# Optimization experiments

Measured on AMD Instinct MI355X. Metric: run time of the kernel, lower is better.

The kernel has to match this reference:

```python
import jax, jax.numpy as jnp
import numpy as np

B, C, H, W = 8, 512, 96, 96
CQ = C // 8


def setup_inputs() -> dict:
    key = jax.random.key(0)
    ks = jax.random.split(key, 8)
    s = 1.0 / np.sqrt(C)  # conv-like init scale to keep logits sane
    return {
        "x": jax.random.normal(ks[0], (B, C, H, W), jnp.float32),
        "Wq": jax.random.normal(ks[1], (CQ, C), jnp.float32) * s,
        "bq": jax.random.normal(ks[2], (CQ,), jnp.float32) * s,
        "Wk": jax.random.normal(ks[3], (CQ, C), jnp.float32) * s,
        "bk": jax.random.normal(ks[4], (CQ,), jnp.float32) * s,
        "Wv": jax.random.normal(ks[5], (C, C), jnp.float32) * s,
        "bv": jax.random.normal(ks[6], (C,), jnp.float32) * s,
        "gamma": jax.random.normal(ks[7], (1,), jnp.float32),
    }


def reference(x, Wq, bq, Wk, bk, Wv, bv, gamma):
    # 1x1 convs == per-pixel linear projections
    q = jnp.einsum('bchw,oc->bohw', x, Wq) + bq[None, :, None, None]  # [B,CQ,H,W]
    k = jnp.einsum('bchw,oc->bohw', x, Wk) + bk[None, :, None, None]  # [B,CQ,H,W]
    v = jnp.einsum('bchw,oc->bohw', x, Wv) + bv[None, :, None, None]  # [B,C ,H,W]

    h = x.shape[2]
    # column (vertical) attention logits: query at (h,w) vs keys at (j,w)
    energy_H = jnp.einsum('bchw,bcjw->bhwj', q, k)  # [B,H,W,H]
    # row (horizontal) attention logits: query at (h,w) vs keys at (h,j)
    energy_W = jnp.einsum('bchw,bchj->bhwj', q, k)  # [B,H,W,W]

    att = jax.nn.softmax(jnp.concatenate([energy_H, energy_W], axis=-1), axis=-1)
    att_H = att[..., :h]   # [B,H,W,H]
    att_W = att[..., h:]   # [B,H,W,W]

    out_H = jnp.einsum('bcjw,bhwj->bchw', v, att_H)
    out_W = jnp.einsum('bchj,bhwj->bchw', v, att_W)
    return gamma[0] * (out_H + out_W)
```

## Files before the change

kernel.cpp:

```cpp
#include <hip/hip_runtime.h>

#define B 8
#define C 512
#define H 96
#define W 96
#define HW (H*W)
#define KD 512
#define NSP 9216

typedef __attribute__((ext_vector_type(4))) float f32x4;
typedef __attribute__((ext_vector_type(8))) _Float16 f16x8;

typedef __attribute__((address_space(3))) unsigned int lds_u32;
typedef const __attribute__((address_space(1))) unsigned int glb_u32;
static __device__ __forceinline__ void gload16(const void* gsrc, void* ldst) {
    __builtin_amdgcn_global_load_lds((glb_u32*)gsrc, (lds_u32*)ldst, 16, 0, 0);
}

static __device__ __forceinline__ int tidx(int row, int kgrp) {
    return row * 32 + ((kgrp ^ ((row >> 2) & 3)) << 3);
}
static __device__ __forceinline__ int tidx64(int row, int gr) {
    return row * 64 + ((gr ^ (row & 7)) << 3);
}

__global__ __launch_bounds__(256) void split_w(
    const float* __restrict__ Wv, const float* __restrict__ Wq, const float* __restrict__ Wk,
    _Float16* __restrict__ Wv_h,
    _Float16* __restrict__ Wqk_h, _Float16* __restrict__ Wqk_l)
{
    int i = blockIdx.x * 256 + threadIdx.x;
    if (i < C * C) Wv_h[i] = (_Float16)Wv[i];
    if (i < 128 * C) {
        int m = i / C, k = i % C;
        float f = (m < 64) ? Wq[m * C + k] : Wk[(m - 64) * C + k];
        _Float16 h = (_Float16)f;
        Wqk_h[i] = h;
        Wqk_l[i] = (_Float16)(f - (float)h);
    }
}

__global__ __launch_bounds__(256) void split_x(
    const float* __restrict__ x,
    _Float16* __restrict__ xhT, _Float16* __restrict__ xlT)
{
    __shared__ float t[64][65];
    int n0 = blockIdx.x * 64, k0 = blockIdx.y * 64, b = blockIdx.z;
    int tid = threadIdx.x;
    const float* xb = x + ((size_t)b * KD + k0) * NSP + n0;
    #pragma unroll
    for (int it = 0; it < 16; ++it) {
        int idx = tid + it * 256;
        t[idx >> 6][idx & 63] = xb[(size_t)(idx >> 6) * NSP + (idx & 63)];
    }
    __syncthreads();
    #pragma unroll
    for (int it = 0; it < 2; ++it) {
        int gid = tid + it * 256;
        int n = gid >> 3, g = gid & 7;
        f16x8 hi, lo;
        #pragma unroll
        for (int u = 0; u < 8; ++u) {
            float f = t[g * 8 + u][n];
            _Float16 hh = (_Float16)f;
            hi[u] = hh;
            lo[u] = (_Float16)(f - (float)hh);
        }
        size_t off = ((size_t)b * NSP + n0 + n) * KD + k0 + g * 8;
        *(f16x8*)&xhT[off] = hi;
        *(f16x8*)&xlT[off] = lo;
    }
}

__global__ __launch_bounds__(256, 2) void gemm_v(
    const _Float16* __restrict__ xhT,
    const _Float16* __restrict__ Wh,
    const float* __restrict__ bias,
    _Float16* __restrict__ out16)
{
    __shared__ _Float16 smem[8192];
    const int W_OFF = 0, X_OFF = 4096;

    int tid = threadIdx.x;
    int n0 = blockIdx.x * 128, m0 = blockIdx.y * 128, b = blockIdx.z;
    int lane = tid & 63, wave = tid >> 6;
    int wr = wave >> 1, wc = wave & 1;
    int l15 = lane & 15, l4 = lane >> 4;

    int grow = tid >> 2, gcol = (tid & 3) * 8;
    const _Float16* pW = Wh + (size_t)(m0 + grow) * KD + gcol;
    const _Float16* pX = xhT + ((size_t)b * NSP + n0 + grow) * KD + gcol;
    const size_t half = (size_t)64 * KD;
    int ldsW0 = W_OFF + wave * 512;
    int ldsW1 = W_OFF + 2048 + wave * 512;
    int ldsX0 = X_OFF + wave * 512;
    int ldsX1 = X_OFF + 2048 + wave * 512;

    f32x4 acc[4][4];
    #pragma unroll
    for (int i = 0; i < 4; ++i)
        #pragma unroll
        for (int j = 0; j < 4; ++j)
            acc[i][j] = (f32x4){0.f, 0.f, 0.f, 0.f};

    for (int k0 = 0; k0 < KD; k0 += 32) {
        gload16(pW + k0,        &smem[ldsW0]);
        gload16(pW + half + k0, &smem[ldsW1]);
        gload16(pX + k0,        &smem[ldsX0]);
        gload16(pX + half + k0, &smem[ldsX1]);
        __syncthreads();

        f16x8 af[4], bf[4];
        #pragma unroll
        for (int f = 0; f < 4; ++f) {
            af[f] = *(const f16x8*)&smem[W_OFF + (wr * 64 + f * 16 + l15) * 32 + l4 * 8];
            bf[f] = *(const f16x8*)&smem[X_OFF + (wc * 64 + f * 16 + l15) * 32 + l4 * 8];
        }
        #pragma unroll
        for (int i = 0; i < 4; ++i)
            #pragma unroll
            for (int j = 0; j < 4; ++j)
                acc[i][j] = __builtin_amdgcn_mfma_f32_16x16x32_f16(af[i], bf[j], acc[i][j], 0, 0, 0);
        __syncthreads();
    }

    #pragma unroll
    for (int i = 0; i < 4; ++i)
        #pragma unroll
        for (int r = 0; r < 4; ++r) {
            int row = m0 + wr * 64 + i * 16 + l4 * 4 + r;
            float bv = bias[row];
            #pragma unroll
            for (int j = 0; j < 4; ++j) {
                int col = n0 + wc * 64 + j * 16 + l15;
                out16[((size_t)b * C + row) * NSP + col] = (_Float16)(acc[i][j][r] + bv);
            }
        }
}

__global__ __launch_bounds__(256, 2) void gemm_qk(
    const _Float16* __restrict__ xhT, const _Float16* __restrict__ xlT,
    const _Float16* __restrict__ Wqh, const _Float16* __restrict__ Wql,
    const float* __restrict__ bias0, const float* __restrict__ bias1,
    _Float16* __restrict__ qh, _Float16* __restrict__ ql,
    _Float16* __restrict__ kh, _Float16* __restrict__ kl)
{
    __shared__ _Float16 smem[16384];
    const int XH = 0, XL = 4096, WHo = 8192, WLo = 12288;

    int tid = threadIdx.x;
    int n0 = blockIdx.x * 128, b = blockIdx.z;
    int lane = tid & 63, wave = tid >> 6;
    int wr = wave >> 1, wc = wave & 1;
    int l15 = lane & 15, l4 = lane >> 4;

    int grow = tid >> 2, gcol = (tid & 3) * 8;
    const _Float16* pXh = xhT + ((size_t)b * NSP + n0 + grow) * KD + gcol;
    const _Float16* pXl = xlT + ((size_t)b * NSP + n0 + grow) * KD + gcol;
    const _Float16* pWh = Wqh + (size_t)grow * KD + gcol;
    const _Float16* pWl = Wql + (size_t)grow * KD + gcol;
    const size_t half = (size_t)64 * KD;
    int base0 = wave * 512, base1 = 2048 + wave * 512;

    f32x4 acc[4][4];
    #pragma unroll
    for (int i = 0; i < 4; ++i)
        #pragma unroll
        for (int j = 0; j < 4; ++j)
            acc[i][j] = (f32x4){0.f, 0.f, 0.f, 0.f};

    for (int k0 = 0; k0 < KD; k0 += 32) {
        gload16(pXh + k0,        &smem[XH + base0]);
        gload16(pXh + half + k0, &smem[XH + base1]);
        gload16(pXl + k0,        &smem[XL + base0]);
        gload16(pXl + half + k0, &smem[XL + base1]);
        gload16(pWh + k0,        &smem[WHo + base0]);
        gload16(pWh + half + k0, &smem[WHo + base1]);
        gload16(pWl + k0,        &smem[WLo + base0]);
        gload16(pWl + half + k0, &smem[WLo + base1]);
        __syncthreads();

        f16x8 axh[4], axl[4], bwh[4], bwl[4];
        #pragma unroll
        for (int f = 0; f < 4; ++f) {
            int ra = (wr * 64 + f * 16 + l15) * 32 + l4 * 8;
            int rb = (wc * 64 + f * 16 + l15) * 32 + l4 * 8;
            axh[f] = *(const f16x8*)&smem[XH + ra];
            axl[f] = *(const f16x8*)&smem[XL + ra];
            bwh[f] = *(const f16x8*)&smem[WHo + rb];
            bwl[f] = *(const f16x8*)&smem[WLo + rb];
        }
        #pragma unroll
        for (int i = 0; i < 4; ++i)
            #pragma unroll
            for (int j = 0; j < 4; ++j)
                acc[i][j] = __builtin_amdgcn_mfma_f32_16x16x32_f16(axh[i], bwh[j], acc[i][j], 0, 0, 0);
        #pragma unroll
        for (int i = 0; i < 4; ++i)
            #pragma unroll
            for (int j = 0; j < 4; ++j)
                acc[i][j] = __builtin_amdgcn_mfma_f32_16x16x32_f16(axh[i], bwl[j], acc[i][j], 0, 0, 0);
        #pragma unroll
        for (int i = 0; i < 4; ++i)
            #pragma unroll
            for (int j = 0; j < 4; ++j)
                acc[i][j] = __builtin_amdgcn_mfma_f32_16x16x32_f16(axl[i], bwh[j], acc[i][j], 0, 0, 0);
        __syncthreads();
    }

    #pragma unroll
    for (int i = 0; i < 4; ++i)
        #pragma unroll
        for (int r = 0; r < 4; ++r) {
            int sp = n0 + wr * 64 + i * 16 + l4 * 4 + r;
            #pragma unroll
            for (int j = 0; j < 4; ++j) {
                int wcol = wc * 64 + j * 16 + l15;
                float val = acc[i][j][r] + (wcol < 64 ? bias0[wcol] : bias1[wcol - 64]);
                _Float16 hi = (_Float16)val;
                _Float16 lo = (_Float16)(val - (float)hi);
                size_t off = ((size_t)b * NSP + sp) * 64 + (wcol & 63);
                if (wcol < 64) { qh[off] = hi; ql[off] = lo; }
                else           { kh[off] = hi; kl[off] = lo; }
            }
        }
}

__global__ __launch_bounds__(256, 2) void energy_mfma(
    const _Float16* __restrict__ qh, const _Float16* __restrict__ ql,
    const _Float16* __restrict__ kh, const _Float16* __restrict__ kl,
    float* __restrict__ out, int pMul, int rMul)
{
    __shared__ _Float16 sm[4 * 96 * 64];
    const int T_QH = 0, T_QL = 6144, T_KH = 12288, T_KL = 18432;
    int p = blockIdx.x, b = blockIdx.y;
    int tid = threadIdx.x;
    size_t base = ((size_t)b * HW + (size_t)p * pMul) * 64;
    size_t rstride = (size_t)rMul * 64;

    #pragma unroll
    for (int tile = 0; tile < 4; ++tile) {
        const _Float16* src = (tile == 0) ? qh : (tile == 1) ? ql : (tile == 2) ? kh : kl;
        int tb = tile * 6144;
        #pragma unroll
        for (int sub = 0; sub < 3; ++sub) {
            int s = sub * 256 + tid;
            int row = s >> 3, g = s & 7;
            f16x8 d = *(const f16x8*)&src[base + row * rstride + g * 8];
            *(f16x8*)&sm[tb + tidx64(row, g)] = d;
        }
    }
    __syncthreads();

    int lane = tid & 63, wave = tid >> 6;
    int wr = wave >> 1, wc = wave & 1;
    int l15 = lane & 15, l4 = lane >> 4;

    f32x4 acc[3][3];
    #pragma unroll
    for (int i = 0; i < 3; ++i)
        #pragma unroll
        for (int j = 0; j < 3; ++j)
            acc[i][j] = (f32x4){0.f, 0.f, 0.f, 0.f};

    #pragma unroll
    for (int ks = 0; ks < 2; ++ks) {
        f16x8 Ah[3], Al[3], Bh[3], Bl[3];
        int gr = ks * 4 + l4;
        #pragma unroll
        for (int i = 0; i < 3; ++i) {
            int sa = tidx64(wr * 48 + i * 16 + l15, gr);
            Ah[i] = *(const f16x8*)&sm[T_QH + sa];
            Al[i] = *(const f16x8*)&sm[T_QL + sa];
            int sb = tidx64(wc * 48 + i * 16 + l15, gr);
            Bh[i] = *(const f16x8*)&sm[T_KH + sb];
            Bl[i] = *(const f16x8*)&sm[T_KL + sb];
        }
        #pragma unroll
        for (int i = 0; i < 3; ++i)
            #pragma unroll
            for (int j = 0; j < 3; ++j) {
                acc[i][j] = __builtin_amdgcn_mfma_f32_16x16x32_f16(Ah[i], Bh[j], acc[i][j], 0, 0, 0);
                acc[i][j] = __builtin_amdgcn_mfma_f32_16x16x32_f16(Ah[i], Bl[j], acc[i][j], 0, 0, 0);
                acc[i][j] = __builtin_amdgcn_mfma_f32_16x16x32_f16(Al[i], Bh[j], acc[i][j], 0, 0, 0);
            }
    }

    size_t ob = (size_t)(b * 96 + p) * 9216;
    #pragma unroll
    for (int i = 0; i < 3; ++i)
        #pragma unroll
        for (int r = 0; r < 4; ++r) {
            int row = wr * 48 + i * 16 + l4 * 4 + r;
            #pragma unroll
            for (int j = 0; j < 3; ++j)
                out[ob + (size_t)row * 96 + wc * 48 + j * 16 + l15] = acc[i][j][r];
        }
}

__global__ __launch_bounds__(256) void maxsum(
    const float* __restrict__ EW, const float* __restrict__ EH,
    const float* __restrict__ gamma, float* __restrict__ ms)
{
    int gw = (blockIdx.x * 256 + threadIdx.x) >> 6;
    int lane = threadIdx.x & 63;
    int b = gw / HW, hw = gw % HW;
    int h = hw / 96, w = hw % 96;
    const float* ew = &EW[((size_t)(b * 96 + h) * 96 + w) * 96];
    const float* eh = &EH[((size_t)(b * 96 + w) * 96 + h) * 96];
    float v0 = ew[lane];
    float v1 = (lane < 32) ? ew[64 + lane] : eh[lane - 32];
    float v2 = eh[32 + lane];
    float m = fmaxf(fmaxf(v0, v1), v2);
    #pragma unroll
    for (int s = 32; s; s >>= 1) m = fmaxf(m, __shfl_xor(m, s));
    float pp = __expf(v0 - m) + __expf(v1 - m) + __expf(v2 - m);
    #pragma unroll
    for (int s = 32; s; s >>= 1) pp += __shfl_xor(pp, s);
    if (lane == 0) {
        ms[(size_t)gw * 2]     = m;
        ms[(size_t)gw * 2 + 1] = gamma[0] / pp;
    }
}

template<int OUT16>
__global__ __launch_bounds__(256) void agg_mfma(
    const float* __restrict__ E, const float* __restrict__ ms,
    const _Float16* __restrict__ v16,
    float* __restrict__ dstF, _Float16* __restrict__ dstH, int msMode)
{
    __shared__ _Float16 satt[3][96 * 32];

    int r = blockIdx.x, b = blockIdx.y;
    int tid = threadIdx.x;
    int lane = tid & 63, wave = tid >> 6;
    int l15 = lane & 15, l4 = lane >> 4;

    const float* Eb = &E[(size_t)(b * 96 + r) * 9216];
    int msBase = b * HW;
    #pragma unroll
    for (int it = 0; it < 5; ++it) {
        int g_id = tid + it * 256;
        if (g_id < 1152) {
            int s = g_id / 12, gj = g_id % 12;
            int mi = msMode ? (msBase + s * 96 + r) : (msBase + r * 96 + s);
            float m  = ms[(size_t)mi * 2];
            float sc = ms[(size_t)mi * 2 + 1];
            float4 e0 = *(const float4*)&Eb[s * 96 + gj * 8];
            float4 e1 = *(const float4*)&Eb[s * 96 + gj * 8 + 4];
            float pv[8] = {e0.x, e0.y, e0.z, e0.w, e1.x, e1.y, e1.z, e1.w};
            f16x8 ph;
            #pragma unroll
            for (int u = 0; u < 8; ++u)
                ph[u] = (_Float16)(__expf(pv[u] - m) * sc);
            *(f16x8*)&satt[gj >> 2][tidx(s, gj & 3)] = ph;
        }
    }
    __syncthreads();

    const _Float16* vb = v16 + (size_t)b * C * 9216 + r * 96;

    for (int cc = 0; cc < 4; ++cc) {
        int cbase = cc * 128 + wave * 32;
        f32x4 acc[2][6];
        #pragma unroll
        for (int i = 0; i < 2; ++i)
            #pragma unroll
            for (int n = 0; n < 6; ++n)
                acc[i][n] = (f32x4){0.f, 0.f, 0.f, 0.f};

        #pragma unroll
        for (int kc = 0; kc < 3; ++kc) {
            f16x8 af[2];
            #pragma unroll
            for (int i = 0; i < 2; ++i)
                af[i] = *(const f16x8*)&vb[(size_t)(cbase + i * 16 + l15) * 9216 + kc * 32 + l4 * 8];
            f16x8 Bp[6];
            #pragma unroll
            for (int n = 0; n < 6; ++n)
                Bp[n] = *(const f16x8*)&satt[kc][tidx(n * 16 + l15, l4)];
            #pragma unroll
            for (int i = 0; i < 2; ++i)
                #pragma unroll
                for (int n = 0; n < 6; ++n)
                    acc[i][n] = __builtin_amdgcn_mfma_f32_16x16x32_f16(af[i], Bp[n], acc[i][n], 0, 0, 0);
        }

        #pragma unroll
        for (int i = 0; i < 2; ++i)
            #pragma unroll
            for (int r4 = 0; r4 < 4; ++r4) {
                int cl = cbase + i * 16 + l4 * 4 + r4;
                size_t rowb = ((size_t)b * C + cl) * 9216 + r * 96;
                #pragma unroll
                for (int n = 0; n < 6; ++n) {
                    int s = n * 16 + l15;
                    if (OUT16) dstH[rowb + s] = (_Float16)acc[i][n][r4];
                    else       dstF[rowb + s] = acc[i][n][r4];
                }
            }
    }
}

__global__ __launch_bounds__(256) void transpose_f16(
    const _Float16* __restrict__ src, _Float16* __restrict__ dst)
{
    size_t base = (size_t)blockIdx.x * (96 * 96);
    __shared__ _Float16 t[96][97];
    int tid = threadIdx.x;
    for (int i = tid; i < 96 * 96; i += 256) t[i / 96][i % 96] = src[base + i];
    __syncthreads();
    for (int i = tid; i < 96 * 96; i += 256) dst[base + i] = t[i % 96][i / 96];
}

__global__ __launch_bounds__(256) void transpose_add(
    const _Float16* __restrict__ srcT, float* __restrict__ out)
{
    size_t base = (size_t)blockIdx.x * (96 * 96);
    __shared__ _Float16 t[96][97];
    int tid = threadIdx.x;
    for (int i = tid; i < 96 * 96; i += 256) t[i / 96][i % 96] = srcT[base + i];
    __syncthreads();
    for (int i = tid; i < 96 * 96; i += 256) out[base + i] += (float)t[i % 96][i / 96];
}

__global__ __launch_bounds__(256) void combine(
    const _Float16* __restrict__ w16, const _Float16* __restrict__ hT,
    float* __restrict__ out)
{
    size_t base = (size_t)blockIdx.x * (96 * 96);
    __shared__ _Float16 t[96][97];
    int tid = threadIdx.x;
    for (int i = tid; i < 96 * 96; i += 256) t[i / 96][i % 96] = hT[base + i];
    __syncthreads();
    for (int i = tid; i < 96 * 96; i += 256)
        out[base + i] = (float)w16[base + i] + (float)t[i % 96][i / 96];
}

extern "C" void kernel_launch(void* const* d_in, const int* in_sizes, int n_in,
                              void* d_out, int out_size, void* d_ws, size_t ws_size,
                              hipStream_t stream)
{
    const float* x     = (const float*)d_in[0];
    const float* Wq    = (const float*)d_in[1];
    const float* bq    = (const float*)d_in[2];
    const float* Wk    = (const float*)d_in[3];
    const float* bk    = (const float*)d_in[4];
    const float* Wv    = (const float*)d_in[5];
    const float* bv    = (const float*)d_in[6];
    const float* gamma = (const float*)d_in[7];
    float* out = (float*)d_out;

    const size_t NK = (size_t)B * NSP * KD;
    _Float16* xhT = (_Float16*)d_ws;
    _Float16* xlT = xhT + NK;
    _Float16* qh  = xlT + NK;
    _Float16* ql  = qh + (size_t)B * HW * 64;
    _Float16* kh  = ql + (size_t)B * HW * 64;
    _Float16* kl  = kh + (size_t)B * HW * 64;
    float* EHp = (float*)(kl + (size_t)B * HW * 64);
    float* EWp = EHp + (size_t)B * HW * 96;
    float* ms  = (float*)qh;
    _Float16* vA  = xlT;
    _Float16* vB  = xhT;
    _Float16* outHT = xlT;

    _Float16* Wv_h  = (_Float16*)EHp;
    _Float16* Wqk_h = Wv_h + (size_t)C * C;
    _Float16* Wqk_l = Wqk_h + (size_t)128 * C;

    const size_t NEED = 245366784ull;
    bool bigws = ws_size >= NEED + NK * sizeof(_Float16);
    _Float16* outW16 = (_Float16*)((char*)d_ws + NEED);

    dim3 blk(256);

    split_w<<<dim3((C*C + 255)/256), blk, 0, stream>>>(Wv, Wq, Wk, Wv_h, Wqk_h, Wqk_l);
    split_x<<<dim3(NSP/64, KD/64, B), blk, 0, stream>>>(x, xhT, xlT);

    gemm_qk<<<dim3(NSP/128, 1, B), blk, 0, stream>>>(xhT, xlT, Wqk_h, Wqk_l, bq, bk, qh, ql, kh, kl);
    gemm_v<<<dim3(NSP/128, C/128, B), blk, 0, stream>>>(xhT, Wv_h, bv, vA);

    energy_mfma<<<dim3(96, B), blk, 0, stream>>>(qh, ql, kh, kl, EWp, 96, 1);
    energy_mfma<<<dim3(96, B), blk, 0, stream>>>(qh, ql, kh, kl, EHp, 1, 96);

    maxsum<<<dim3(B*HW/4), blk, 0, stream>>>(EWp, EHp, gamma, ms);

    transpose_f16<<<dim3(B*C), blk, 0, stream>>>(vA, vB);

    if (bigws) {
        agg_mfma<1><<<dim3(96, B), blk, 0, stream>>>(EWp, ms, vA, nullptr, outW16, 0);
        agg_mfma<1><<<dim3(96, B), blk, 0, stream>>>(EHp, ms, vB, nullptr, outHT, 1);
        combine<<<dim3(B*C), blk, 0, stream>>>(outW16, outHT, out);
    } else {
        agg_mfma<0><<<dim3(96, B), blk, 0, stream>>>(EWp, ms, vA, out, nullptr, 0);
        agg_mfma<1><<<dim3(96, B), blk, 0, stream>>>(EHp, ms, vB, nullptr, outHT, 1);
        transpose_add<<<dim3(B*C), blk, 0, stream>>>(outHT, out);
    }
}
```

Before: 382.1 us.

## Fuse softmax max/sum partials into energy kernel and vectorize split_x loads

```diff
diff --git a/kernel.cpp b/kernel.cpp
--- a/kernel.cpp
+++ b/kernel.cpp
@@ -49,9 +49,14 @@
     int tid = threadIdx.x;
     const float* xb = x + ((size_t)b * KD + k0) * NSP + n0;
     #pragma unroll
-    for (int it = 0; it < 16; ++it) {
+    for (int it = 0; it < 4; ++it) {
         int idx = tid + it * 256;
-        t[idx >> 6][idx & 63] = xb[(size_t)(idx >> 6) * NSP + (idx & 63)];
+        int kr = idx >> 4, nq = idx & 15;
+        float4 v = *(const float4*)&xb[(size_t)kr * NSP + nq * 4];
+        t[kr][nq * 4 + 0] = v.x;
+        t[kr][nq * 4 + 1] = v.y;
+        t[kr][nq * 4 + 2] = v.z;
+        t[kr][nq * 4 + 3] = v.w;
     }
     __syncthreads();
     #pragma unroll
@@ -229,7 +234,7 @@
 __global__ __launch_bounds__(256, 2) void energy_mfma(
     const _Float16* __restrict__ qh, const _Float16* __restrict__ ql,
     const _Float16* __restrict__ kh, const _Float16* __restrict__ kl,
-    float* __restrict__ out, int pMul, int rMul)
+    float* __restrict__ out, float* __restrict__ part, int pMul, int rMul)
 {
     __shared__ _Float16 sm[4 * 96 * 64];
     const int T_QH = 0, T_QL = 6144, T_KH = 12288, T_KL = 18432;
@@ -296,31 +301,49 @@
             for (int j = 0; j < 3; ++j)
                 out[ob + (size_t)row * 96 + wc * 48 + j * 16 + l15] = acc[i][j][r];
         }
-}
-
-__global__ __launch_bounds__(256) void maxsum(
-    const float* __restrict__ EW, const float* __restrict__ EH,
+
+    __syncthreads();
+    float* scr = (float*)sm;
+    #pragma unroll
+    for (int i = 0; i < 3; ++i)
+        #pragma unroll
+        for (int r = 0; r < 4; ++r) {
+            int row = wr * 48 + i * 16 + l4 * 4 + r;
+            float m3 = fmaxf(fmaxf(acc[i][0][r], acc[i][1][r]), acc[i][2][r]);
+            #pragma unroll
+            for (int mk = 1; mk < 16; mk <<= 1) m3 = fmaxf(m3, __shfl_xor(m3, mk));
+            float s = __expf(acc[i][0][r] - m3) + __expf(acc[i][1][r] - m3) + __expf(acc[i][2][r] - m3);
+            #pragma unroll
+            for (int mk = 1; mk < 16; mk <<= 1) s += __shfl_xor(s, mk);
+            if (l15 == 0) {
+                scr[row * 4 + wc * 2]     = m3;
+                scr[row * 4 + wc * 2 + 1] = s;
+            }
+        }
+    __syncthreads();
+    if (tid < 96) {
+        float m0 = scr[tid * 4], s0 = scr[tid * 4 + 1];
+        float m1 = scr[tid * 4 + 2], s1 = scr[tid * 4 + 3];
+        float M = fmaxf(m0, m1);
+        float S = s0 * __expf(m0 - M) + s1 * __expf(m1 - M);
+        size_t idx = (pMul == 96) ? ((size_t)b * HW + p * 96 + tid)
+                                  : ((size_t)b * HW + tid * 96 + p);
+        part[idx * 2]     = M;
+        part[idx * 2 + 1] = S;
+    }
+}
+
+__global__ __launch_bounds__(256) void combine_ms(
+    const float* __restrict__ pW, const float* __restrict__ pH,
     const float* __restrict__ gamma, float* __restrict__ ms)
 {
-    int gw = (blockIdx.x * 256 + threadIdx.x) >> 6;
-    int lane = threadIdx.x & 63;
-    int b = gw / HW, hw = gw % HW;
-    int h = hw / 96, w = hw % 96;
-    const float* ew = &EW[((size_t)(b * 96 + h) * 96 + w) * 96];
-    const float* eh = &EH[((size_t)(b * 96 + w) * 96 + h) * 96];
-    float v0 = ew[lane];
-    float v1 = (lane < 32) ? ew[64 + lane] : eh[lane - 32];
-    float v2 = eh[32 + lane];
-    float m = fmaxf(fmaxf(v0, v1), v2);
-    #pragma unroll
-    for (int s = 32; s; s >>= 1) m = fmaxf(m, __shfl_xor(m, s));
-    float pp = __expf(v0 - m) + __expf(v1 - m) + __expf(v2 - m);
-    #pragma unroll
-    for (int s = 32; s; s >>= 1) pp += __shfl_xor(pp, s);
-    if (lane == 0) {
-        ms[(size_t)gw * 2]     = m;
-        ms[(size_t)gw * 2 + 1] = gamma[0] / pp;
-    }
+    int row = blockIdx.x * 256 + threadIdx.x;
+    float mW = pW[row * 2], sW = pW[row * 2 + 1];
+    float mH = pH[row * 2], sH = pH[row * 2 + 1];
+    float M = fmaxf(mW, mH);
+    float S = sW * __expf(mW - M) + sH * __expf(mH - M);
+    ms[row * 2]     = M;
+    ms[row * 2 + 1] = gamma[0] / S;
 }
 
 template<int OUT16>
@@ -464,6 +487,8 @@
     _Float16* vA  = xlT;
     _Float16* vB  = xhT;
     _Float16* outHT = xlT;
+    float* pW = (float*)xhT;
+    float* pH = pW + (size_t)2 * B * HW;
 
     _Float16* Wv_h  = (_Float16*)EHp;
     _Float16* Wqk_h = Wv_h + (size_t)C * C;
@@ -481,10 +506,9 @@
     gemm_qk<<<dim3(NSP/128, 1, B), blk, 0, stream>>>(xhT, xlT, Wqk_h, Wqk_l, bq, bk, qh, ql, kh, kl);
     gemm_v<<<dim3(NSP/128, C/128, B), blk, 0, stream>>>(xhT, Wv_h, bv, vA);
 
-    energy_mfma<<<dim3(96, B), blk, 0, stream>>>(qh, ql, kh, kl, EWp, 96, 1);
-    energy_mfma<<<dim3(96, B), blk, 0, stream>>>(qh, ql, kh, kl, EHp, 1, 96);
-
-    maxsum<<<dim3(B*HW/4), blk, 0, stream>>>(EWp, EHp, gamma, ms);
+    energy_mfma<<<dim3(96, B), blk, 0, stream>>>(qh, ql, kh, kl, EWp, pW, 96, 1);
+    energy_mfma<<<dim3(96, B), blk, 0, stream>>>(qh, ql, kh, kl, EHp, pH, 1, 96);
+    combine_ms<<<dim3(B*HW/256), blk, 0, stream>>>(pW, pH, gamma, ms);
 
     transpose_f16<<<dim3(B*C), blk, 0, stream>>>(vA, vB);
 
```

Result: no change. 378.2 us (-1.0%).
